# Performance work log

Measured on AMD Instinct MI355X. Metric: run time of the kernel, lower is better.

Reference implementation:

```python
import jax, jax.numpy as jnp
import numpy as np

BATCH = 1 << 20
ACT_BIT, WEIGHT_BIT, BIAS_BIT = 16, 8, 32


def _sym_scale(x_min, x_max, bits):
    # symmetric_linear_quantization_params: scale = max(|min|,|max|) / (2^(b-1)-1)
    n = float(2 ** (bits - 1) - 1)
    s = jnp.maximum(jnp.abs(x_min), jnp.abs(x_max)) / n
    return jax.lax.stop_gradient(jnp.maximum(s, 1e-8))


def _quant_int(x, scale, bits):
    # SymmetricQuantFunction with straight-through estimator: returns integer-valued array
    n = 2 ** (bits - 1) - 1
    y = x / scale
    q = jnp.clip(jnp.round(y), -n - 1, n)
    return y + jax.lax.stop_gradient(q - y)


def quant_act(x, bits=ACT_BIT):
    # QuantAct: dynamic per-tensor symmetric quantize -> dequantize
    scale = _sym_scale(jnp.min(x), jnp.max(x), bits)
    x_int = _quant_int(x, scale, bits)
    return x_int * scale, scale


def quant_linear(x_deq, act_scale, W, b):
    # QuantLinear: per-output-channel int8 weights, int32 bias with scale = w_scale*act_scale,
    # integer matmul then dequant by bias_scale. Returns (float out, per-channel w scale).
    w_scale = _sym_scale(jnp.min(W, axis=1), jnp.max(W, axis=1), WEIGHT_BIT)  # [out]
    w_int = _quant_int(W, w_scale[:, None], WEIGHT_BIT)                        # [out, in]
    bias_scale = w_scale * act_scale                                           # [out]
    b_int = _quant_int(b, bias_scale, BIAS_BIT)                                # [out]
    x_int = x_deq / act_scale                                                  # [B, in]
    out = (jnp.einsum('bi,oi->bo', x_int, w_int) + b_int) * bias_scale
    return out, w_scale


def setup_inputs() -> dict:
    key = jax.random.key(0)
    ks = jax.random.split(key, 9)
    dims = [(64, 16), (32, 64), (32, 32), (5, 32)]
    inp = {"x": jax.random.normal(ks[0], (BATCH, 16), dtype=jnp.float32)}
    for i, (o, c) in enumerate(dims, start=1):
        inp[f"W{i}"] = jax.random.normal(ks[2 * i - 1], (o, c), dtype=jnp.float32) * (1.0 / np.sqrt(c))
        inp[f"b{i}"] = jax.random.normal(ks[2 * i], (o,), dtype=jnp.float32) * 0.01
    return inp


def reference(x, W1, b1, W2, b2, W3, b3, W4, b4):
    h, a_scale = quant_act(x)
    h, _ = quant_linear(h, a_scale, W1, b1)
    h = jax.nn.relu(h)
    h, a_scale = quant_act(h)
    h, _ = quant_linear(h, a_scale, W2, b2)
    h = jax.nn.relu(h)
    h, a_scale = quant_act(h)
    h, _ = quant_linear(h, a_scale, W3, b3)
    h = jax.nn.relu(h)
    h, a_scale = quant_act(h)
    h, _ = quant_linear(h, a_scale, W4, b4)
    return jax.nn.softmax(h, axis=1)
```

## Files before the change

### kernel.cpp

```cpp
#include <hip/hip_runtime.h>
#include <math.h>

#define DEV __device__ __forceinline__

typedef short s16x8 __attribute__((ext_vector_type(8)));
typedef float f32x4 __attribute__((ext_vector_type(4)));

static constexpr int W1S = 16;
static constexpr int W2S = 80;
static constexpr int W3S = 112;
static constexpr int W4S = 144;
static constexpr int F0  = 256;

DEV float qbias(float b, float bs) {
    float q = rintf(b / bs);
    return fminf(fmaxf(q, -2.147483648e9f), 2.147483648e9f);
}

DEV unsigned short bf16b(float f) {
    return (unsigned short)(__float_as_uint(f) >> 16);
}

DEV void reduceAndAtomicMax(float v, unsigned int* slot) {
    #pragma unroll
    for (int off = 32; off; off >>= 1) v = fmaxf(v, __shfl_xor(v, off));
    __shared__ float sm[16];
    const int wid = threadIdx.x >> 6;
    if ((threadIdx.x & 63) == 0) sm[wid] = v;
    __syncthreads();
    if (threadIdx.x == 0) {
        const int nw = blockDim.x >> 6;
        float m = sm[0];
        for (int i = 1; i < nw; i++) m = fmaxf(m, sm[i]);
        atomicMax(slot, __float_as_uint(m));
    }
}

__global__ __launch_bounds__(256) void k_quantw(const float* __restrict__ W1,
                                                const float* __restrict__ W2,
                                                const float* __restrict__ W3,
                                                const float* __restrict__ W4,
                                                float* __restrict__ wsf) {
    __shared__ int wq1[64 * 16], wq2[32 * 64], wq3[32 * 32], wq4[5 * 32];
    int* wsi = (int*)wsf;
    const int t = threadIdx.x;
    if (t < 4) ((unsigned int*)wsf)[t] = 0u;

    const float* W = nullptr; int row = -1, cols = 0; int* dq = nullptr; float* dsc = nullptr;
    if (t < 64)       { W = W1; row = t;       cols = 16; dq = wq1 + row * 16; dsc = wsf + W1S + row; }
    else if (t < 96)  { W = W2; row = t - 64;  cols = 64; dq = wq2 + row * 64; dsc = wsf + W2S + row; }
    else if (t < 128) { W = W3; row = t - 96;  cols = 32; dq = wq3 + row * 32; dsc = wsf + W3S + row; }
    else if (t < 133) { W = W4; row = t - 128; cols = 32; dq = wq4 + row * 32; dsc = wsf + W4S + row; }
    if (row >= 0) {
        const float* src = W + row * cols;
        float m = 0.f;
        for (int i = 0; i < cols; i++) m = fmaxf(m, fabsf(src[i]));
        float s = fmaxf(m * (1.0f / 127.0f), 1e-8f);
        *dsc = s;
        for (int i = 0; i < cols; i++) {
            float q = fminf(fmaxf(rintf(src[i] / s), -128.f), 127.f);
            dq[i] = (int)q;
        }
    }
    __syncthreads();

    for (int sIdx = t; sIdx < 18 * 64; sIdx += 256) {
        const int f = sIdx >> 6, l = sIdx & 63;
        const int grp = l >> 4, li = l & 15;
        int dw[4];
        #pragma unroll
        for (int d = 0; d < 4; d++) {
            unsigned int hv[2];
            #pragma unroll
            for (int h = 0; h < 2; h++) {
                const int e = 2 * d + h;
                int wv;
                if (f < 4) {
                    wv = wq1[(f * 16 + li) * 16 + (grp & 1) * 8 + e];
                } else if (f < 12) {
                    int mt = (f - 4) >> 2, c = (f - 4) & 3;
                    wv = wq2[(mt * 16 + li) * 64 + 16 * c + 4 * grp + (e & 3)];
                } else if (f < 16) {
                    int mt = (f - 12) >> 1, c = (f - 12) & 1;
                    wv = wq3[(mt * 16 + li) * 32 + 16 * c + 4 * grp + (e & 3)];
                } else {
                    int c = f - 16;
                    wv = (li < 5) ? wq4[li * 32 + 16 * c + 4 * grp + (e & 3)] : 0;
                }
                hv[h] = bf16b((float)wv);
            }
            dw[d] = (int)(hv[0] | (hv[1] << 16));
        }
        ((int4*)(wsi + F0))[f * 64 + l] = make_int4(dw[0], dw[1], dw[2], dw[3]);
    }
}

__global__ __launch_bounds__(1024, 4) void k_absmax(const float4* __restrict__ x,
                                                    unsigned int* __restrict__ slots, int n4) {
    float m = 0.f;
    for (int i = blockIdx.x * blockDim.x + threadIdx.x; i < n4; i += gridDim.x * blockDim.x) {
        float4 v = x[i];
        m = fmaxf(m, fmaxf(fmaxf(fabsf(v.x), fabsf(v.y)), fmaxf(fabsf(v.z), fabsf(v.w))));
    }
    reduceAndAtomicMax(m, slots + 0);
}

DEV int packhi(float q0, float q1) {
    return (int)__builtin_amdgcn_perm(__float_as_uint(q1), __float_as_uint(q0), 0x07060302u);
}

DEV void qsplit2(float a0, float a1, float2 c0, float2 c1, int& hw, int& lw) {
    float t0 = fmaf(a0, c0.x, c0.y);
    float t1 = fmaf(a1, c1.x, c1.y);
    float q0 = fmaxf(rintf(t0), 0.f);
    float q1 = fmaxf(rintf(t1), 0.f);
    float h0 = __uint_as_float(__float_as_uint(q0) & 0xFFFF0000u);
    float h1 = __uint_as_float(__float_as_uint(q1) & 0xFFFF0000u);
    hw = packhi(h0, h1);
    lw = packhi(q0 - h0, q1 - h1);
}

DEV s16x8 mkfrag(f32x4 acc, const float2* cq) {
    int h01, h23, l01, l23;
    qsplit2(acc[0], acc[1], cq[0], cq[1], h01, l01);
    qsplit2(acc[2], acc[3], cq[2], cq[3], h23, l23);
    return __builtin_bit_cast(s16x8, make_int4(h01, h23, l01, l23));
}

DEV float qxsel(float v, float inv0, bool hi) {
    float q = rintf(v * inv0);
    float h = __uint_as_float(__float_as_uint(q) & 0xFFFF0000u);
    return hi ? h : (q - h);
}

template <int STAGE, int WPB_, int TPW_>
DEV void stage_body(const float* __restrict__ x,
                    const float* __restrict__ b1, const float* __restrict__ b2,
                    const float* __restrict__ b3, const float* __restrict__ b4,
                    const float* __restrict__ wsf, unsigned int* __restrict__ slots,
                    float* __restrict__ out) {
    __shared__ float2 QA[64], QB[32], QC[32], QD[16];
    const int t = threadIdx.x;
    const int w = t >> 6, l = t & 63;
    const int grp = l >> 4, li = l & 15;

    const float s0 = fmaxf(__uint_as_float(slots[0]) * (1.f / 32767.f), 1e-8f);
    float s1 = 1.f, s2 = 1.f, s3 = 1.f;
    if (STAGE >= 2) s1 = fmaxf(__uint_as_float(slots[1]) * (1.f / 32767.f), 1e-8f);
    if (STAGE >= 3) s2 = fmaxf(__uint_as_float(slots[2]) * (1.f / 32767.f), 1e-8f);
    if (STAGE >= 4) s3 = fmaxf(__uint_as_float(slots[3]) * (1.f / 32767.f), 1e-8f);
    const float inv0 = 1.f / s0;
    const float inv1 = (STAGE >= 2) ? 1.f / s1 : 0.f;
    const float inv2 = (STAGE >= 3) ? 1.f / s2 : 0.f;
    const float inv3 = (STAGE >= 4) ? 1.f / s3 : 0.f;

    if (t < 64) {
        float bs = wsf[W1S + t] * s0; float bi = qbias(b1[t], bs) * bs;
        QA[t] = (STAGE == 1) ? make_float2(bs, bi) : make_float2(bs * inv1, bi * inv1);
    }
    if (STAGE >= 2 && t >= 64 && t < 96) {
        int i = t - 64;
        float bs = wsf[W2S + i] * s1; float bi = qbias(b2[i], bs) * bs;
        QB[i] = (STAGE == 2) ? make_float2(bs, bi) : make_float2(bs * inv2, bi * inv2);
    }
    if (STAGE >= 3 && t >= 96 && t < 128) {
        int i = t - 96;
        float bs = wsf[W3S + i] * s2; float bi = qbias(b3[i], bs) * bs;
        QC[i] = (STAGE == 3) ? make_float2(bs, bi) : make_float2(bs * inv3, bi * inv3);
    }
    if (STAGE >= 4 && t >= 128 && t < 144) {
        int i = t - 128;
        if (i < 5) { float bs = wsf[W4S + i] * s3; QD[i] = make_float2(bs, qbias(b4[i], bs) * bs); }
        else QD[i] = make_float2(0.f, 0.f);
    }
    __syncthreads();

    const int4* fr = (const int4*)((const int*)wsf + F0);
    s16x8 A1[4], A2[2][4], A3[2][2], A4[2];
    #pragma unroll
    for (int nt = 0; nt < 4; nt++) A1[nt] = __builtin_bit_cast(s16x8, fr[nt * 64 + l]);
    if (STAGE >= 2)
        #pragma unroll
        for (int mt = 0; mt < 2; mt++)
            #pragma unroll
            for (int c = 0; c < 4; c++) A2[mt][c] = __builtin_bit_cast(s16x8, fr[(4 + mt * 4 + c) * 64 + l]);
    if (STAGE >= 3)
        #pragma unroll
        for (int mt = 0; mt < 2; mt++)
            #pragma unroll
            for (int c = 0; c < 2; c++) A3[mt][c] = __builtin_bit_cast(s16x8, fr[(12 + mt * 2 + c) * 64 + l]);
    if (STAGE >= 4) {
        A4[0] = __builtin_bit_cast(s16x8, fr[16 * 64 + l]);
        A4[1] = __builtin_bit_cast(s16x8, fr[17 * 64 + l]);
    }

    float2 cq1[4][4], cq2[2][4], cq3[2][4], e4[4];
    if (STAGE >= 2)
        #pragma unroll
        for (int nt = 0; nt < 4; nt++)
            #pragma unroll
            for (int r = 0; r < 4; r++) cq1[nt][r] = QA[16 * nt + 4 * grp + r];
    if (STAGE >= 3)
        #pragma unroll
        for (int mt = 0; mt < 2; mt++)
            #pragma unroll
            for (int r = 0; r < 4; r++) cq2[mt][r] = QB[16 * mt + 4 * grp + r];
    if (STAGE >= 4) {
        #pragma unroll
        for (int mt = 0; mt < 2; mt++)
            #pragma unroll
            for (int r = 0; r < 4; r++) cq3[mt][r] = QC[16 * mt + 4 * grp + r];
        #pragma unroll
        for (int r = 0; r < 4; r++) e4[r] = QD[4 * grp + r];
    }

    float ma1[4][4], ma2[2][4], ma3[2][4];
    if (STAGE == 1)
        #pragma unroll
        for (int nt = 0; nt < 4; nt++)
            #pragma unroll
            for (int r = 0; r < 4; r++) ma1[nt][r] = -3.402823466e38f;
    if (STAGE == 2)
        #pragma unroll
        for (int mt = 0; mt < 2; mt++)
            #pragma unroll
            for (int r = 0; r < 4; r++) ma2[mt][r] = -3.402823466e38f;
    if (STAGE == 3)
        #pragma unroll
        for (int mt = 0; mt < 2; mt++)
            #pragma unroll
            for (int r = 0; r < 4; r++) ma3[mt][r] = -3.402823466e38f;

    const bool hiLane = (grp < 2);
    const size_t tile0 = ((size_t)blockIdx.x * WPB_ + w) * (size_t)TPW_;

    float4 px0, px1;
    {
        const float4* xr = (const float4*)(x + (tile0 * 16 + li) * 16 + (grp & 1) * 8);
        px0 = xr[0]; px1 = xr[1];
    }

    for (int it = 0; it < TPW_; ++it) {
        const size_t row0 = (tile0 + it) * 16;
        float4 v0 = px0, v1 = px1;
        if (it + 1 < TPW_) {
            const float4* xr = (const float4*)(x + ((tile0 + it + 1) * 16 + li) * 16 + (grp & 1) * 8);
            px0 = xr[0]; px1 = xr[1];
        }

        s16x8 b1v;
        {
            float p0 = qxsel(v0.x, inv0, hiLane), p1 = qxsel(v0.y, inv0, hiLane);
            float p2 = qxsel(v0.z, inv0, hiLane), p3 = qxsel(v0.w, inv0, hiLane);
            float p4 = qxsel(v1.x, inv0, hiLane), p5 = qxsel(v1.y, inv0, hiLane);
            float p6 = qxsel(v1.z, inv0, hiLane), p7 = qxsel(v1.w, inv0, hiLane);
            b1v = __builtin_bit_cast(s16x8,
                make_int4(packhi(p0, p1), packhi(p2, p3), packhi(p4, p5), packhi(p6, p7)));
        }

        s16x8 B2f[4];
        #pragma unroll
        for (int nt = 0; nt < 4; nt++) {
            f32x4 acc = {0.f, 0.f, 0.f, 0.f};
            acc = __builtin_amdgcn_mfma_f32_16x16x32_bf16(A1[nt], b1v, acc, 0, 0, 0);
            if constexpr (STAGE == 1) {
                #pragma unroll
                for (int r = 0; r < 4; r++) ma1[nt][r] = fmaxf(ma1[nt][r], acc[r]);
            } else {
                B2f[nt] = mkfrag(acc, cq1[nt]);
            }
        }
        if constexpr (STAGE == 1) continue;

        f32x4 acc2[2] = {{0.f, 0.f, 0.f, 0.f}, {0.f, 0.f, 0.f, 0.f}};
        #pragma unroll
        for (int c = 0; c < 4; c++) {
            acc2[0] = __builtin_amdgcn_mfma_f32_16x16x32_bf16(A2[0][c], B2f[c], acc2[0], 0, 0, 0);
            acc2[1] = __builtin_amdgcn_mfma_f32_16x16x32_bf16(A2[1][c], B2f[c], acc2[1], 0, 0, 0);
        }
        if constexpr (STAGE == 2) {
            #pragma unroll
            for (int mt = 0; mt < 2; mt++)
                #pragma unroll
                for (int r = 0; r < 4; r++) ma2[mt][r] = fmaxf(ma2[mt][r], acc2[mt][r]);
            continue;
        }

        if constexpr (STAGE >= 3) {
            s16x8 B3f[2];
            #pragma unroll
            for (int c = 0; c < 2; c++) B3f[c] = mkfrag(acc2[c], cq2[c]);

            f32x4 acc3[2] = {{0.f, 0.f, 0.f, 0.f}, {0.f, 0.f, 0.f, 0.f}};
            #pragma unroll
            for (int c = 0; c < 2; c++) {
                acc3[0] = __builtin_amdgcn_mfma_f32_16x16x32_bf16(A3[0][c], B3f[c], acc3[0], 0, 0, 0);
                acc3[1] = __builtin_amdgcn_mfma_f32_16x16x32_bf16(A3[1][c], B3f[c], acc3[1], 0, 0, 0);
            }
            if constexpr (STAGE == 3) {
                #pragma unroll
                for (int mt = 0; mt < 2; mt++)
                    #pragma unroll
                    for (int r = 0; r < 4; r++) ma3[mt][r] = fmaxf(ma3[mt][r], acc3[mt][r]);
                continue;
            }

            if constexpr (STAGE == 4) {
                s16x8 B4f[2];
                #pragma unroll
                for (int c = 0; c < 2; c++) B4f[c] = mkfrag(acc3[c], cq3[c]);

                f32x4 acc4 = {0.f, 0.f, 0.f, 0.f};
                acc4 = __builtin_amdgcn_mfma_f32_16x16x32_bf16(A4[0], B4f[0], acc4, 0, 0, 0);
                acc4 = __builtin_amdgcn_mfma_f32_16x16x32_bf16(A4[1], B4f[1], acc4, 0, 0, 0);

                float lg0 = fmaf(acc4[0], e4[0].x, e4[0].y);
                float lg1 = fmaf(acc4[1], e4[1].x, e4[1].y);
                float lg2 = fmaf(acc4[2], e4[2].x, e4[2].y);
                float lg3 = fmaf(acc4[3], e4[3].x, e4[3].y);
                float lg4 = __shfl(lg0, li + 16);

                if (l < 16) {
                    float m = fmaxf(fmaxf(fmaxf(lg0, lg1), fmaxf(lg2, lg3)), lg4);
                    float e0 = __expf(lg0 - m), e1 = __expf(lg1 - m), e2 = __expf(lg2 - m),
                          e3 = __expf(lg3 - m), ee4 = __expf(lg4 - m);
                    float r = 1.f / (e0 + e1 + e2 + e3 + ee4);
                    float* dst = out + (row0 + l) * 5;
                    dst[0] = e0 * r; dst[1] = e1 * r; dst[2] = e2 * r; dst[3] = e3 * r; dst[4] = ee4 * r;
                }
            }
        }
    }

    if (STAGE == 1) {
        float vmax = 0.f;
        #pragma unroll
        for (int nt = 0; nt < 4; nt++)
            #pragma unroll
            for (int r = 0; r < 4; r++) {
                float2 c = QA[16 * nt + 4 * grp + r];
                vmax = fmaxf(vmax, fmaf(ma1[nt][r], c.x, c.y));
            }
        reduceAndAtomicMax(vmax, slots + 1);
    } else if (STAGE == 2) {
        float vmax = 0.f;
        #pragma unroll
        for (int mt = 0; mt < 2; mt++)
            #pragma unroll
            for (int r = 0; r < 4; r++) {
                float2 c = QB[16 * mt + 4 * grp + r];
                vmax = fmaxf(vmax, fmaf(ma2[mt][r], c.x, c.y));
            }
        reduceAndAtomicMax(vmax, slots + 2);
    } else if (STAGE == 3) {
        float vmax = 0.f;
        #pragma unroll
        for (int mt = 0; mt < 2; mt++)
            #pragma unroll
            for (int r = 0; r < 4; r++) {
                float2 c = QC[16 * mt + 4 * grp + r];
                vmax = fmaxf(vmax, fmaf(ma3[mt][r], c.x, c.y));
            }
        reduceAndAtomicMax(vmax, slots + 3);
    }
}

__global__ __launch_bounds__(1024, 4) void k_s1(const float* x, const float* b1, const float* b2,
                                                const float* b3, const float* b4, const float* ws,
                                                unsigned int* slots, float* out) {
    stage_body<1, 16, 8>(x, b1, b2, b3, b4, ws, slots, out);
}
__global__ __launch_bounds__(1024, 4) void k_s2(const float* x, const float* b1, const float* b2,
                                                const float* b3, const float* b4, const float* ws,
                                                unsigned int* slots, float* out) {
    stage_body<2, 16, 8>(x, b1, b2, b3, b4, ws, slots, out);
}
__global__ __launch_bounds__(512, 2) void k_s3(const float* x, const float* b1, const float* b2,
                                               const float* b3, const float* b4, const float* ws,
                                               unsigned int* slots, float* out) {
    stage_body<3, 8, 16>(x, b1, b2, b3, b4, ws, slots, out);
}
__global__ __launch_bounds__(512, 2) void k_s4(const float* x, const float* b1, const float* b2,
                                               const float* b3, const float* b4, const float* ws,
                                               unsigned int* slots, float* out) {
    stage_body<4, 8, 16>(x, b1, b2, b3, b4, ws, slots, out);
}

extern "C" void kernel_launch(void* const* d_in, const int* in_sizes, int n_in,
                              void* d_out, int out_size, void* d_ws, size_t ws_size,
                              hipStream_t stream) {
    const float* x  = (const float*)d_in[0];
    const float* W1 = (const float*)d_in[1];
    const float* b1 = (const float*)d_in[2];
    const float* W2 = (const float*)d_in[3];
    const float* b2 = (const float*)d_in[4];
    const float* W3 = (const float*)d_in[5];
    const float* b3 = (const float*)d_in[6];
    const float* W4 = (const float*)d_in[7];
    const float* b4 = (const float*)d_in[8];
    float* out = (float*)d_out;
    float* ws = (float*)d_ws;
    unsigned int* slots = (unsigned int*)d_ws;

    const int B = in_sizes[0] / 16;
    const int blocks12 = B / (16 * 8 * 16);
    const int blocks34 = B / (8 * 16 * 16);

    k_quantw<<<1, 256, 0, stream>>>(W1, W2, W3, W4, ws);
    k_absmax<<<512, 1024, 0, stream>>>((const float4*)x, slots, in_sizes[0] / 4);
    k_s1<<<blocks12, 1024, 0, stream>>>(x, b1, b2, b3, b4, ws, slots, out);
    k_s2<<<blocks12, 1024, 0, stream>>>(x, b1, b2, b3, b4, ws, slots, out);
    k_s3<<<blocks34, 512, 0, stream>>>(x, b1, b2, b3, b4, ws, slots, out);
    k_s4<<<blocks34, 512, 0, stream>>>(x, b1, b2, b3, b4, ws, slots, out);
}
```

Measured before the change: 163.2 us.

## Fuse absmax and four MLP stages into one cooperative persistent kernel

Replaces the five back-to-back launches (absmax plus four recompute stages) with a single cooperative kernel that runs the same phases separated by grid-wide syncs, using a persistent grid-stride tile loop. Scale slots are read with agent-scope atomic loads so later phases see the maxima produced earlier. This aims to remove per-launch gaps and tail effects, at the cost of grid-sync overhead, a fixed 512-thread block size for every phase, and occupancy queries on the host each call. The old multi-kernel path is kept as a fallback if the cooperative launch fails.

```diff
diff --git a/kernel.cpp b/kernel.cpp
--- a/kernel.cpp
+++ b/kernel.cpp
@@ -1,7 +1,10 @@
 #include <hip/hip_runtime.h>
+#include <hip/hip_cooperative_groups.h>
 #include <math.h>
 
 #define DEV __device__ __forceinline__
+
+namespace cg = cooperative_groups;
 
 typedef short s16x8 __attribute__((ext_vector_type(8)));
 typedef float f32x4 __attribute__((ext_vector_type(4)));
@@ -34,6 +37,12 @@
         for (int i = 1; i < nw; i++) m = fmaxf(m, sm[i]);
         atomicMax(slot, __float_as_uint(m));
     }
+    __syncthreads();
+}
+
+DEV float ldscale(const unsigned int* p) {
+    unsigned u = __hip_atomic_load(p, __ATOMIC_RELAXED, __HIP_MEMORY_SCOPE_AGENT);
+    return fmaxf(__uint_as_float(u) * (1.f / 32767.f), 1e-8f);
 }
 
 __global__ __launch_bounds__(256) void k_quantw(const float* __restrict__ W1,
@@ -95,16 +104,6 @@
     }
 }
 
-__global__ __launch_bounds__(1024, 4) void k_absmax(const float4* __restrict__ x,
-                                                    unsigned int* __restrict__ slots, int n4) {
-    float m = 0.f;
-    for (int i = blockIdx.x * blockDim.x + threadIdx.x; i < n4; i += gridDim.x * blockDim.x) {
-        float4 v = x[i];
-        m = fmaxf(m, fmaxf(fmaxf(fabsf(v.x), fabsf(v.y)), fmaxf(fabsf(v.z), fabsf(v.w))));
-    }
-    reduceAndAtomicMax(m, slots + 0);
-}
-
 DEV int packhi(float q0, float q1) {
     return (int)__builtin_amdgcn_perm(__float_as_uint(q1), __float_as_uint(q0), 0x07060302u);
 }
@@ -133,22 +132,22 @@
     return hi ? h : (q - h);
 }
 
-template <int STAGE, int WPB_, int TPW_>
-DEV void stage_body(const float* __restrict__ x,
+template <int STAGE>
+DEV void phase_body(const float* __restrict__ x,
                     const float* __restrict__ b1, const float* __restrict__ b2,
                     const float* __restrict__ b3, const float* __restrict__ b4,
                     const float* __restrict__ wsf, unsigned int* __restrict__ slots,
-                    float* __restrict__ out) {
+                    float* __restrict__ out, int nTiles, int waveId, int totalWaves) {
     __shared__ float2 QA[64], QB[32], QC[32], QD[16];
     const int t = threadIdx.x;
-    const int w = t >> 6, l = t & 63;
+    const int l = t & 63;
     const int grp = l >> 4, li = l & 15;
 
-    const float s0 = fmaxf(__uint_as_float(slots[0]) * (1.f / 32767.f), 1e-8f);
+    const float s0 = ldscale(slots + 0);
     float s1 = 1.f, s2 = 1.f, s3 = 1.f;
-    if (STAGE >= 2) s1 = fmaxf(__uint_as_float(slots[1]) * (1.f / 32767.f), 1e-8f);
-    if (STAGE >= 3) s2 = fmaxf(__uint_as_float(slots[2]) * (1.f / 32767.f), 1e-8f);
-    if (STAGE >= 4) s3 = fmaxf(__uint_as_float(slots[3]) * (1.f / 32767.f), 1e-8f);
+    if (STAGE >= 2) s1 = ldscale(slots + 1);
+    if (STAGE >= 3) s2 = ldscale(slots + 2);
+    if (STAGE >= 4) s3 = ldscale(slots + 3);
     const float inv0 = 1.f / s0;
     const float inv1 = (STAGE >= 2) ? 1.f / s1 : 0.f;
     const float inv2 = (STAGE >= 3) ? 1.f / s2 : 0.f;
@@ -232,21 +231,21 @@
             for (int r = 0; r < 4; r++) ma3[mt][r] = -3.402823466e38f;
 
     const bool hiLane = (grp < 2);
-    const size_t tile0 = ((size_t)blockIdx.x * WPB_ + w) * (size_t)TPW_;
-
-    float4 px0, px1;
-    {
-        const float4* xr = (const float4*)(x + (tile0 * 16 + li) * 16 + (grp & 1) * 8);
+
+    float4 px0 = {0.f, 0.f, 0.f, 0.f}, px1 = {0.f, 0.f, 0.f, 0.f};
+    int tile = waveId;
+    if (tile < nTiles) {
+        const float4* xr = (const float4*)(x + ((size_t)tile * 16 + li) * 16 + (grp & 1) * 8);
         px0 = xr[0]; px1 = xr[1];
     }
-
-    for (int it = 0; it < TPW_; ++it) {
-        const size_t row0 = (tile0 + it) * 16;
+    for (; tile < nTiles; tile += totalWaves) {
         float4 v0 = px0, v1 = px1;
-        if (it + 1 < TPW_) {
-            const float4* xr = (const float4*)(x + ((tile0 + it + 1) * 16 + li) * 16 + (grp & 1) * 8);
+        const int nxt = tile + totalWaves;
+        if (nxt < nTiles) {
+            const float4* xr = (const float4*)(x + ((size_t)nxt * 16 + li) * 16 + (grp & 1) * 8);
             px0 = xr[0]; px1 = xr[1];
         }
+        const size_t row0 = (size_t)tile * 16;
 
         s16x8 b1v;
         {
@@ -365,25 +364,76 @@
     }
 }
 
+__global__ __launch_bounds__(512, 2) void k_fused(const float* __restrict__ x,
+                                                  const float* __restrict__ b1,
+                                                  const float* __restrict__ b2,
+                                                  const float* __restrict__ b3,
+                                                  const float* __restrict__ b4,
+                                                  const float* __restrict__ wsf,
+                                                  unsigned int* __restrict__ slots,
+                                                  float* __restrict__ out,
+                                                  int nTiles, int n4) {
+    cg::grid_group gg = cg::this_grid();
+    const int t = threadIdx.x;
+    const int waveId = blockIdx.x * 8 + (t >> 6);
+    const int totalWaves = gridDim.x * 8;
+
+    {
+        float m = 0.f;
+        const float4* xv = (const float4*)x;
+        const int stride = gridDim.x * 512;
+        for (int i = blockIdx.x * 512 + t; i < n4; i += stride) {
+            float4 v = xv[i];
+            m = fmaxf(m, fmaxf(fmaxf(fabsf(v.x), fabsf(v.y)), fmaxf(fabsf(v.z), fabsf(v.w))));
+        }
+        reduceAndAtomicMax(m, slots + 0);
+    }
+    gg.sync();
+    phase_body<1>(x, b1, b2, b3, b4, wsf, slots, out, nTiles, waveId, totalWaves);
+    gg.sync();
+    phase_body<2>(x, b1, b2, b3, b4, wsf, slots, out, nTiles, waveId, totalWaves);
+    gg.sync();
+    phase_body<3>(x, b1, b2, b3, b4, wsf, slots, out, nTiles, waveId, totalWaves);
+    gg.sync();
+    phase_body<4>(x, b1, b2, b3, b4, wsf, slots, out, nTiles, waveId, totalWaves);
+}
+
+__global__ __launch_bounds__(1024, 4) void k_absmax(const float4* __restrict__ x,
+                                                    unsigned int* __restrict__ slots, int n4) {
+    float m = 0.f;
+    for (int i = blockIdx.x * blockDim.x + threadIdx.x; i < n4; i += gridDim.x * blockDim.x) {
+        float4 v = x[i];
+        m = fmaxf(m, fmaxf(fmaxf(fabsf(v.x), fabsf(v.y)), fmaxf(fabsf(v.z), fabsf(v.w))));
+    }
+    reduceAndAtomicMax(m, slots + 0);
+}
+
+template <int STAGE, int WPB_, int TPW_>
+DEV void stage_fixed(const float* x, const float* b1, const float* b2, const float* b3,
+                     const float* b4, const float* wsf, unsigned int* slots, float* out) {
+    const int waveId = blockIdx.x * WPB_ + (threadIdx.x >> 6);
+    phase_body<STAGE>(x, b1, b2, b3, b4, wsf, slots, out, 65536, waveId, gridDim.x * WPB_);
+}
+
 __global__ __launch_bounds__(1024, 4) void k_s1(const float* x, const float* b1, const float* b2,
                                                 const float* b3, const float* b4, const float* ws,
                                                 unsigned int* slots, float* out) {
-    stage_body<1, 16, 8>(x, b1, b2, b3, b4, ws, slots, out);
+    stage_fixed<1, 16, 8>(x, b1, b2, b3, b4, ws, slots, out);
 }
 __global__ __launch_bounds__(1024, 4) void k_s2(const float* x, const float* b1, const float* b2,
                                                 const float* b3, const float* b4, const float* ws,
                                                 unsigned int* slots, float* out) {
-    stage_body<2, 16, 8>(x, b1, b2, b3, b4, ws, slots, out);
+    stage_fixed<2, 16, 8>(x, b1, b2, b3, b4, ws, slots, out);
 }
 __global__ __launch_bounds__(512, 2) void k_s3(const float* x, const float* b1, const float* b2,
                                                const float* b3, const float* b4, const float* ws,
                                                unsigned int* slots, float* out) {
-    stage_body<3, 8, 16>(x, b1, b2, b3, b4, ws, slots, out);
+    stage_fixed<3, 8, 16>(x, b1, b2, b3, b4, ws, slots, out);
 }
 __global__ __launch_bounds__(512, 2) void k_s4(const float* x, const float* b1, const float* b2,
                                                const float* b3, const float* b4, const float* ws,
                                                unsigned int* slots, float* out) {
-    stage_body<4, 8, 16>(x, b1, b2, b3, b4, ws, slots, out);
+    stage_fixed<4, 8, 16>(x, b1, b2, b3, b4, ws, slots, out);
 }
 
 extern "C" void kernel_launch(void* const* d_in, const int* in_sizes, int n_in,
@@ -403,13 +453,33 @@
     unsigned int* slots = (unsigned int*)d_ws;
 
     const int B = in_sizes[0] / 16;
-    const int blocks12 = B / (16 * 8 * 16);
-    const int blocks34 = B / (8 * 16 * 16);
+    int nTiles = B / 16;
+    int n4 = in_sizes[0] / 4;
 
     k_quantw<<<1, 256, 0, stream>>>(W1, W2, W3, W4, ws);
-    k_absmax<<<512, 1024, 0, stream>>>((const float4*)x, slots, in_sizes[0] / 4);
-    k_s1<<<blocks12, 1024, 0, stream>>>(x, b1, b2, b3, b4, ws, slots, out);
-    k_s2<<<blocks12, 1024, 0, stream>>>(x, b1, b2, b3, b4, ws, slots, out);
-    k_s3<<<blocks34, 512, 0, stream>>>(x, b1, b2, b3, b4, ws, slots, out);
-    k_s4<<<blocks34, 512, 0, stream>>>(x, b1, b2, b3, b4, ws, slots, out);
-}
+
+    int dev = 0;
+    (void)hipGetDevice(&dev);
+    int nCU = 256;
+    (void)hipDeviceGetAttribute(&nCU, hipDeviceAttributeMultiprocessorCount, dev);
+    int bpc = 0;
+    hipError_t qe = hipOccupancyMaxActiveBlocksPerMultiprocessor(&bpc, k_fused, 512, 0);
+    bool tryCoop = (qe == hipSuccess && bpc >= 1);
+    hipError_t e = hipErrorUnknown;
+    if (tryCoop) {
+        if (bpc > 2) bpc = 2;
+        int gridB = nCU * bpc;
+        if (gridB > 512) gridB = 512;
+        const float* xp = x;
+        void* args[] = {(void*)&xp, (void*)&b1, (void*)&b2, (void*)&b3, (void*)&b4,
+                        (void*)&ws, (void*)&slots, (void*)&out, (void*)&nTiles, (void*)&n4};
+        e = hipLaunchCooperativeKernel((void*)k_fused, dim3(gridB), dim3(512), args, 0, stream);
+    }
+    if (e != hipSuccess) {
+        k_absmax<<<512, 1024, 0, stream>>>((const float4*)x, slots, n4);
+        k_s1<<<512, 1024, 0, stream>>>(x, b1, b2, b3, b4, ws, slots, out);
+        k_s2<<<512, 1024, 0, stream>>>(x, b1, b2, b3, b4, ws, slots, out);
+        k_s3<<<512, 512, 0, stream>>>(x, b1, b2, b3, b4, ws, slots, out);
+        k_s4<<<512, 512, 0, stream>>>(x, b1, b2, b3, b4, ws, slots, out);
+    }
+}
```

Result: slower. 176.7 us (+8.3%).
